# Kernel optimization log

Measured on AMD Instinct MI355X. Metric: run time of the kernel, lower is better.

Reference implementation:

```python
import jax, jax.numpy as jnp
import numpy as np

L = 2048
E = 1024
H = 16
D = E // H


def setup_inputs() -> dict:
    key = jax.random.key(0)
    ks = jax.random.split(key, 9)
    inp = {
        "values": jax.random.normal(ks[0], (L, E), dtype=jnp.float32),
        "keys": jax.random.normal(ks[1], (L, E), dtype=jnp.float32),
        "query": jax.random.normal(ks[2], (L, E), dtype=jnp.float32),
        "dist_matrix": jax.random.uniform(ks[3], (L, L), dtype=jnp.float32),
        "Wv": jax.random.normal(ks[4], (E, E), dtype=jnp.float32) * 0.02,
        "Wk": jax.random.normal(ks[5], (E, E), dtype=jnp.float32) * 0.02,
        "Wq": jax.random.normal(ks[6], (E, E), dtype=jnp.float32) * 0.02,
        "Wo": jax.random.normal(ks[7], (E, E), dtype=jnp.float32) * 0.02,
        "bo": jax.random.normal(ks[8], (E,), dtype=jnp.float32) * 0.02,
    }
    return inp


def reference(values, keys, query, dist_matrix, Wv, Wk, Wq, Wo, bo):
    # Linear projections (torch Linear: x @ W.T), then split heads: [L, H, D]
    v = (values @ Wv.T).reshape(L, H, D)
    k = (keys @ Wk.T).reshape(L, H, D)
    q = (query @ Wq.T).reshape(L, H, D)

    # energy: [H, Lq, Lk]
    energy = jnp.einsum("qhd,khd->hqk", q, k)

    # distance bias: zeros -> inf, then 1/(d+1); broadcast over heads
    dm = jnp.where(dist_matrix == 0, jnp.inf, dist_matrix)
    bias = 1.0 / (dm + 1.0)
    energy = energy + bias[None, :, :]

    attn = jax.nn.softmax(energy / jnp.sqrt(jnp.float32(E)), axis=2)

    out = jnp.einsum("hql,lhd->qhd", attn, v).reshape(L, H * D)
    return out @ Wo.T + bo
```

## Files before the change

### kernel.cpp

```cpp
#include <hip/hip_runtime.h>


#define L_SEQ 2048
#define E_DIM 1024
#define H_HEADS 16
#define D_HEAD 64
#define KSPLIT 4

typedef unsigned short u16;
typedef __attribute__((ext_vector_type(8))) short bf16x8;
typedef __attribute__((ext_vector_type(8))) unsigned short u16x8;
typedef __attribute__((ext_vector_type(4))) unsigned short u16x4;
typedef __attribute__((ext_vector_type(4))) float f32x4;

__device__ __forceinline__ float bf2f(u16 u) {
  union { unsigned int i; float f; } v; v.i = ((unsigned int)u) << 16; return v.f;
}
__device__ __forceinline__ u16 f2bf(float f) {
  union { float f; unsigned int i; } v; v.f = f;
  unsigned int u = v.i;
  u += 0x7FFFu + ((u >> 16) & 1u);
  return (u16)(u >> 16);
}

__global__ void cvt_all(const float* __restrict__ xq, const float* __restrict__ xk,
                        const float* __restrict__ xv,
                        const float* __restrict__ wq, const float* __restrict__ wk,
                        const float* __restrict__ wv, const float* __restrict__ wo,
                        const float* __restrict__ dist,
                        u16* oq, u16* ok, u16* ov,
                        u16* owq, u16* owk, u16* owv, u16* owo, u16* obias)
{
  size_t gid = (size_t)blockIdx.x * 256 + threadIdx.x;
  const size_t NQ = 524288;
  const size_t NW = 262144;
  const float* src; u16* dst; size_t off; bool isb = false;
  if      (gid <     NQ)           { src = xq;   dst = oq;    off = gid; }
  else if (gid < 2 * NQ)           { src = xk;   dst = ok;    off = gid - NQ; }
  else if (gid < 3 * NQ)           { src = xv;   dst = ov;    off = gid - 2 * NQ; }
  else if (gid < 3 * NQ + NW)      { src = wq;   dst = owq;   off = gid - 3 * NQ; }
  else if (gid < 3 * NQ + 2 * NW)  { src = wk;   dst = owk;   off = gid - 3 * NQ - NW; }
  else if (gid < 3 * NQ + 3 * NW)  { src = wv;   dst = owv;   off = gid - 3 * NQ - 2 * NW; }
  else if (gid < 3 * NQ + 4 * NW)  { src = wo;   dst = owo;   off = gid - 3 * NQ - 3 * NW; }
  else { src = dist; dst = obias; off = gid - 3 * NQ - 4 * NW; isb = true; }

  f32x4 v = *(const f32x4*)&src[off * 4];
  u16x4 o;
#pragma unroll
  for (int j = 0; j < 4; ++j) {
    float f = v[j];
    if (isb) f = (f == 0.f) ? 0.f : 1.f / (f + 1.f);
    o[j] = f2bf(f);
  }
  *(u16x4*)&dst[off * 4] = o;
}

#define TM 128
#define TN 128
#define BK 32
#define LDK 40

template<int OUTMODE>
__global__ __launch_bounds__(256, 2) void gemm_bt3b(
    const u16* __restrict__ A0, const u16* __restrict__ B0, void* __restrict__ C0,
    const u16* __restrict__ A1, const u16* __restrict__ B1, void* __restrict__ C1,
    const u16* __restrict__ A2, const u16* __restrict__ B2, void* __restrict__ C2,
    const float* __restrict__ bias, int M, int N, int K)
{
  const u16* A; const u16* B; void* C;
  if (blockIdx.z == 0)      { A = A0; B = B0; C = C0; }
  else if (blockIdx.z == 1) { A = A1; B = B1; C = C1; }
  else                      { A = A2; B = B2; C = C2; }

  __shared__ __align__(16) u16 As[TM][LDK];
  __shared__ __align__(16) u16 Bs[TN][LDK];

  const int m0 = blockIdx.y * TM;
  const int n0 = blockIdx.x * TN;
  const int t = threadIdx.x;
  const int wave = t >> 6;
  const int lane = t & 63;
  const int quad = lane >> 4;
  const int col  = lane & 15;
  const int wm = (wave >> 1) * 64;
  const int wn = (wave & 1) * 64;

  f32x4 acc[4][4];
#pragma unroll
  for (int i = 0; i < 4; ++i)
#pragma unroll
    for (int j = 0; j < 4; ++j) acc[i][j] = (f32x4){0.f, 0.f, 0.f, 0.f};

  for (int k0 = 0; k0 < K; k0 += BK) {
    __syncthreads();
#pragma unroll
    for (int s = 0; s < 2; ++s) {
      int idx = t + s * 256;
      int r  = idx >> 2;
      int c8 = (idx & 3) * 8;
      *(u16x8*)&As[r][c8] = *(const u16x8*)&A[(size_t)(m0 + r) * K + k0 + c8];
      *(u16x8*)&Bs[r][c8] = *(const u16x8*)&B[(size_t)(n0 + r) * K + k0 + c8];
    }
    __syncthreads();

    bf16x8 af[4], bfr[4];
#pragma unroll
    for (int i = 0; i < 4; ++i)
      af[i] = *(const bf16x8*)&As[wm + i * 16 + col][quad * 8];
#pragma unroll
    for (int j = 0; j < 4; ++j)
      bfr[j] = *(const bf16x8*)&Bs[wn + j * 16 + col][quad * 8];

#pragma unroll
    for (int i = 0; i < 4; ++i)
#pragma unroll
      for (int j = 0; j < 4; ++j)
        acc[i][j] = __builtin_amdgcn_mfma_f32_16x16x32_bf16(af[i], bfr[j], acc[i][j], 0, 0, 0);
  }

  const bool transC = (OUTMODE == 0) && (blockIdx.z == 2);
#pragma unroll
  for (int i = 0; i < 4; ++i) {
    int rowb = m0 + wm + i * 16 + quad * 4;
#pragma unroll
    for (int j = 0; j < 4; ++j) {
      int cn = n0 + wn + j * 16 + col;
      if (OUTMODE == 1) {
        float badd = bias ? bias[cn] : 0.f;
#pragma unroll
        for (int r = 0; r < 4; ++r)
          ((float*)C)[(size_t)(rowb + r) * N + cn] = acc[i][j][r] + badd;
      } else if (transC) {
        u16x4 pk;
#pragma unroll
        for (int r = 0; r < 4; ++r) pk[r] = f2bf(acc[i][j][r]);
        *(u16x4*)&((u16*)C)[(size_t)cn * M + rowb] = pk;
      } else {
#pragma unroll
        for (int r = 0; r < 4; ++r)
          ((u16*)C)[(size_t)(rowb + r) * N + cn] = f2bf(acc[i][j][r]);
      }
    }
  }
}

#define FK 64
#define LDV 72

__global__ __launch_bounds__(256, 5) void flash2(
    const u16* __restrict__ Q, const u16* __restrict__ Kp,
    const u16* __restrict__ Vt, const u16* __restrict__ Bb,
    u16* __restrict__ Op, float* __restrict__ lp)
{
  __shared__ __align__(16) u16 Ks[FK][LDV];
  __shared__ __align__(16) u16 Vs[D_HEAD][LDV];
  __shared__ __align__(16) u16 Ps[4][16][LDV];

  const int h  = blockIdx.y;
  const int q0 = blockIdx.x * 64;
  const int z  = blockIdx.z;
  const int hoff = h * D_HEAD;
  const int kbase = z * (L_SEQ / KSPLIT);
  const int t = threadIdx.x;
  const int wave = t >> 6;
  const int lane = t & 63;
  const int quad = lane >> 4;
  const int col  = lane & 15;

  bf16x8 qf[2];
  {
    const u16* qrow = Q + (size_t)(q0 + wave * 16 + col) * E_DIM + hoff;
    qf[0] = *(const bf16x8*)(qrow + quad * 8);
    qf[1] = *(const bf16x8*)(qrow + 32 + quad * 8);
  }

  float l_lane[4] = {0.f, 0.f, 0.f, 0.f};
  f32x4 oacc[4];
#pragma unroll
  for (int td = 0; td < 4; ++td) oacc[td] = (f32x4){0.f, 0.f, 0.f, 0.f};

  const int qrow_mine = q0 + wave * 16 + quad * 4;

  const int cst = t & 7, rst = t >> 3;
  for (int kt = 0; kt < L_SEQ / KSPLIT / FK; ++kt) {
    const int k0 = kbase + kt * FK;
    __syncthreads();
#pragma unroll
    for (int s = 0; s < 2; ++s) {
      int rr = rst + s * 32;
      *(u16x8*)&Ks[rr][cst * 8] = *(const u16x8*)&Kp[(size_t)(k0 + rr) * E_DIM + hoff + cst * 8];
      *(u16x8*)&Vs[rr][cst * 8] = *(const u16x8*)&Vt[(size_t)(hoff + rr) * L_SEQ + k0 + cst * 8];
    }
    float bias_v[4][4];
#pragma unroll
    for (int tt = 0; tt < 4; ++tt)
#pragma unroll
      for (int r = 0; r < 4; ++r)
        bias_v[tt][r] = bf2f(Bb[(size_t)(qrow_mine + r) * L_SEQ + k0 + tt * 16 + col]);
    __syncthreads();

    f32x4 sacc[4];
#pragma unroll
    for (int tt = 0; tt < 4; ++tt) {
      f32x4 a = (f32x4){0.f, 0.f, 0.f, 0.f};
      a = __builtin_amdgcn_mfma_f32_16x16x32_bf16(qf[0], *(const bf16x8*)&Ks[tt * 16 + col][quad * 8], a, 0, 0, 0);
      a = __builtin_amdgcn_mfma_f32_16x16x32_bf16(qf[1], *(const bf16x8*)&Ks[tt * 16 + col][32 + quad * 8], a, 0, 0, 0);
      sacc[tt] = a;
    }

#pragma unroll
    for (int tt = 0; tt < 4; ++tt) {
#pragma unroll
      for (int r = 0; r < 4; ++r) {
        float p = __expf((sacc[tt][r] + bias_v[tt][r]) * 0.03125f);
        l_lane[r] += p;
        Ps[wave][quad * 4 + r][tt * 16 + col] = f2bf(p);
      }
    }

#pragma unroll
    for (int kk = 0; kk < 2; ++kk) {
      bf16x8 pf = *(const bf16x8*)&Ps[wave][col][kk * 32 + quad * 8];
#pragma unroll
      for (int td = 0; td < 4; ++td) {
        bf16x8 vf = *(const bf16x8*)&Vs[td * 16 + col][kk * 32 + quad * 8];
        oacc[td] = __builtin_amdgcn_mfma_f32_16x16x32_bf16(pf, vf, oacc[td], 0, 0, 0);
      }
    }
  }

#pragma unroll
  for (int off = 1; off < 16; off <<= 1)
#pragma unroll
    for (int r = 0; r < 4; ++r) l_lane[r] += __shfl_xor(l_lane[r], off);

#pragma unroll
  for (int td = 0; td < 4; ++td)
#pragma unroll
    for (int r = 0; r < 4; ++r)
      Op[((size_t)z * L_SEQ + qrow_mine + r) * E_DIM + hoff + td * 16 + col] = f2bf(oacc[td][r]);

  if (col == 0) {
#pragma unroll
    for (int r = 0; r < 4; ++r)
      lp[((size_t)z * L_SEQ + qrow_mine + r) * H_HEADS + h] = l_lane[r];
  }
}

__global__ void merge_attn(const u16* __restrict__ Op, const float* __restrict__ lp,
                           u16* __restrict__ AOb)
{
  size_t gid = (size_t)blockIdx.x * 256 + threadIdx.x;
  size_t idx = gid * 4;
  int q = (int)(idx >> 10);
  int e = (int)(idx & 1023);
  int h = e >> 6;
  float o[4] = {0.f, 0.f, 0.f, 0.f};
  float lsum = 0.f;
#pragma unroll
  for (int s = 0; s < KSPLIT; ++s) {
    u16x4 pv = *(const u16x4*)&Op[((size_t)s * L_SEQ + q) * E_DIM + e];
#pragma unroll
    for (int j = 0; j < 4; ++j) o[j] += bf2f(pv[j]);
    lsum += lp[((size_t)s * L_SEQ + q) * H_HEADS + h];
  }
  float inv = 1.f / lsum;
  u16x4 pk;
#pragma unroll
  for (int j = 0; j < 4; ++j) pk[j] = f2bf(o[j] * inv);
  *(u16x4*)&AOb[idx] = pk;
}

extern "C" void kernel_launch(void* const* d_in, const int* in_sizes, int n_in,
                              void* d_out, int out_size, void* d_ws, size_t ws_size,
                              hipStream_t stream)
{
  const float* values = (const float*)d_in[0];
  const float* keys   = (const float*)d_in[1];
  const float* query  = (const float*)d_in[2];
  const float* dist   = (const float*)d_in[3];
  const float* Wv     = (const float*)d_in[4];
  const float* Wk     = (const float*)d_in[5];
  const float* Wq     = (const float*)d_in[6];
  const float* Wo     = (const float*)d_in[7];
  const float* bo     = (const float*)d_in[8];
  float* out = (float*)d_out;

  const size_t MB = (size_t)1 << 20;
  char* w = (char*)d_ws;
  u16* xq  = (u16*)(w + 0 * MB);
  u16* xk  = (u16*)(w + 4 * MB);
  u16* xv  = (u16*)(w + 8 * MB);
  u16* wqb = (u16*)(w + 12 * MB);
  u16* wkb = (u16*)(w + 14 * MB);
  u16* wvb = (u16*)(w + 16 * MB);
  u16* wob = (u16*)(w + 18 * MB);
  u16* Bb  = (u16*)(w + 20 * MB);
  u16* Qh  = (u16*)(w + 28 * MB);
  u16* Kh  = (u16*)(w + 32 * MB);
  u16* Vth = (u16*)(w + 36 * MB);
  u16* AOb = (u16*)(w + 40 * MB);
  float* lp = (float*)(w + 44 * MB);
  u16* Op  = (u16*)(w + 0 * MB);

  cvt_all<<<14336, 256, 0, stream>>>(query, keys, values, Wq, Wk, Wv, Wo, dist,
                                     xq, xk, xv, wqb, wkb, wvb, wob, Bb);

  dim3 gProj(E_DIM / TN, L_SEQ / TM, 3);
  gemm_bt3b<0><<<gProj, 256, 0, stream>>>(xq, wqb, Qh,
                                          xk, wkb, Kh,
                                          xv, wvb, Vth,
                                          nullptr, L_SEQ, E_DIM, E_DIM);

  dim3 gAttn(L_SEQ / 64, H_HEADS, KSPLIT);
  flash2<<<gAttn, 256, 0, stream>>>(Qh, Kh, Vth, Bb, Op, lp);

  merge_attn<<<(L_SEQ * E_DIM / 4) / 256, 256, 0, stream>>>(Op, lp, AOb);

  dim3 gOut(E_DIM / TN, L_SEQ / TM, 1);
  gemm_bt3b<1><<<gOut, 256, 0, stream>>>(AOb, wob, out,
                                         AOb, wob, out,
                                         AOb, wob, out,
                                         bo, L_SEQ, E_DIM, E_DIM);
}
```

Measured before the change: 236.1 us.

## Use direct global-to-LDS loads in GEMM and transpose score layout in attention

The projection GEMM now stages A/B tiles with global_load_lds directly into unpadded shared memory, avoiding a register round-trip. The attention kernel swaps MFMA operands so each lane holds one query row, which allows vectorized bias loads, packed bf16 stores of P and a single row-sum register per lane. Exponentials become exp2 with log2e folded into the precomputed bias and a fused multiply-add. Removing the LDS padding may bring back bank conflicts on the fragment reads, and the packing uses a simpler rounding.

```diff
diff --git a/kernel.cpp b/kernel.cpp
--- a/kernel.cpp
+++ b/kernel.cpp
@@ -8,19 +8,32 @@
 #define KSPLIT 4
 
 typedef unsigned short u16;
+typedef unsigned int u32;
 typedef __attribute__((ext_vector_type(8))) short bf16x8;
 typedef __attribute__((ext_vector_type(8))) unsigned short u16x8;
 typedef __attribute__((ext_vector_type(4))) unsigned short u16x4;
 typedef __attribute__((ext_vector_type(4))) float f32x4;
 
+#define C_LOG2E_32 0.045084220027780106f
+
 __device__ __forceinline__ float bf2f(u16 u) {
-  union { unsigned int i; float f; } v; v.i = ((unsigned int)u) << 16; return v.f;
+  union { u32 i; float f; } v; v.i = ((u32)u) << 16; return v.f;
 }
 __device__ __forceinline__ u16 f2bf(float f) {
-  union { float f; unsigned int i; } v; v.f = f;
-  unsigned int u = v.i;
+  union { float f; u32 i; } v; v.f = f;
+  u32 u = v.i;
   u += 0x7FFFu + ((u >> 16) & 1u);
   return (u16)(u >> 16);
+}
+__device__ __forceinline__ u32 pack_bf16_pair(float lo, float hi) {
+  union { float f; u32 u; } a, b;
+  a.f = lo; b.f = hi;
+  return __builtin_amdgcn_perm(b.u + 0x8000u, a.u + 0x8000u, 0x07060302u);
+}
+__device__ __forceinline__ void gload16(const u16* g, u16* l) {
+  __builtin_amdgcn_global_load_lds(
+      (const __attribute__((address_space(1))) u32*)g,
+      (__attribute__((address_space(3))) u32*)l, 16, 0, 0);
 }
 
 __global__ void cvt_all(const float* __restrict__ xq, const float* __restrict__ xk,
@@ -49,7 +62,7 @@
 #pragma unroll
   for (int j = 0; j < 4; ++j) {
     float f = v[j];
-    if (isb) f = (f == 0.f) ? 0.f : 1.f / (f + 1.f);
+    if (isb) f = (f == 0.f) ? 0.f : C_LOG2E_32 / (f + 1.f);
     o[j] = f2bf(f);
   }
   *(u16x4*)&dst[off * 4] = o;
@@ -58,7 +71,6 @@
 #define TM 128
 #define TN 128
 #define BK 32
-#define LDK 40
 
 template<int OUTMODE>
 __global__ __launch_bounds__(256, 2) void gemm_bt3b(
@@ -72,8 +84,8 @@
   else if (blockIdx.z == 1) { A = A1; B = B1; C = C1; }
   else                      { A = A2; B = B2; C = C2; }
 
-  __shared__ __align__(16) u16 As[TM][LDK];
-  __shared__ __align__(16) u16 Bs[TN][LDK];
+  __shared__ __align__(16) u16 As[TM][BK];
+  __shared__ __align__(16) u16 Bs[TN][BK];
 
   const int m0 = blockIdx.y * TM;
   const int n0 = blockIdx.x * TN;
@@ -85,6 +97,15 @@
   const int wm = (wave >> 1) * 64;
   const int wn = (wave & 1) * 64;
 
+  const int lr = lane >> 2;
+  const int lc = (lane & 3) * 8;
+  const u16* gA = A + (size_t)(m0 + wave * 32 + lr) * K + lc;
+  const u16* gB = B + (size_t)(n0 + wave * 32 + lr) * K + lc;
+  u16* lA0 = &As[wave * 32][0];
+  u16* lA1 = &As[wave * 32 + 16][0];
+  u16* lB0 = &Bs[wave * 32][0];
+  u16* lB1 = &Bs[wave * 32 + 16][0];
+
   f32x4 acc[4][4];
 #pragma unroll
   for (int i = 0; i < 4; ++i)
@@ -93,14 +114,10 @@
 
   for (int k0 = 0; k0 < K; k0 += BK) {
     __syncthreads();
-#pragma unroll
-    for (int s = 0; s < 2; ++s) {
-      int idx = t + s * 256;
-      int r  = idx >> 2;
-      int c8 = (idx & 3) * 8;
-      *(u16x8*)&As[r][c8] = *(const u16x8*)&A[(size_t)(m0 + r) * K + k0 + c8];
-      *(u16x8*)&Bs[r][c8] = *(const u16x8*)&B[(size_t)(n0 + r) * K + k0 + c8];
-    }
+    gload16(gA + k0, lA0);
+    gload16(gA + (size_t)16 * K + k0, lA1);
+    gload16(gB + k0, lB0);
+    gload16(gB + (size_t)16 * K + k0, lB1);
     __syncthreads();
 
     bf16x8 af[4], bfr[4];
@@ -147,7 +164,7 @@
 #define FK 64
 #define LDV 72
 
-__global__ __launch_bounds__(256, 5) void flash2(
+__global__ __launch_bounds__(256, 5) void flash3(
     const u16* __restrict__ Q, const u16* __restrict__ Kp,
     const u16* __restrict__ Vt, const u16* __restrict__ Bb,
     u16* __restrict__ Op, float* __restrict__ lp)
@@ -174,14 +191,14 @@
     qf[1] = *(const bf16x8*)(qrow + 32 + quad * 8);
   }
 
-  float l_lane[4] = {0.f, 0.f, 0.f, 0.f};
+  float l_lane = 0.f;
   f32x4 oacc[4];
 #pragma unroll
   for (int td = 0; td < 4; ++td) oacc[td] = (f32x4){0.f, 0.f, 0.f, 0.f};
 
-  const int qrow_mine = q0 + wave * 16 + quad * 4;
-
+  const u16* brow = Bb + (size_t)(q0 + wave * 16 + col) * L_SEQ;
   const int cst = t & 7, rst = t >> 3;
+
   for (int kt = 0; kt < L_SEQ / KSPLIT / FK; ++kt) {
     const int k0 = kbase + kt * FK;
     __syncthreads();
@@ -191,31 +208,30 @@
       *(u16x8*)&Ks[rr][cst * 8] = *(const u16x8*)&Kp[(size_t)(k0 + rr) * E_DIM + hoff + cst * 8];
       *(u16x8*)&Vs[rr][cst * 8] = *(const u16x8*)&Vt[(size_t)(hoff + rr) * L_SEQ + k0 + cst * 8];
     }
-    float bias_v[4][4];
-#pragma unroll
-    for (int tt = 0; tt < 4; ++tt)
-#pragma unroll
-      for (int r = 0; r < 4; ++r)
-        bias_v[tt][r] = bf2f(Bb[(size_t)(qrow_mine + r) * L_SEQ + k0 + tt * 16 + col]);
+    float pb[4][4];
+#pragma unroll
+    for (int tt = 0; tt < 4; ++tt) {
+      u16x4 bv = *(const u16x4*)&brow[k0 + tt * 16 + quad * 4];
+#pragma unroll
+      for (int r = 0; r < 4; ++r) pb[tt][r] = bf2f(bv[r]);
+    }
     __syncthreads();
 
-    f32x4 sacc[4];
 #pragma unroll
     for (int tt = 0; tt < 4; ++tt) {
       f32x4 a = (f32x4){0.f, 0.f, 0.f, 0.f};
-      a = __builtin_amdgcn_mfma_f32_16x16x32_bf16(qf[0], *(const bf16x8*)&Ks[tt * 16 + col][quad * 8], a, 0, 0, 0);
-      a = __builtin_amdgcn_mfma_f32_16x16x32_bf16(qf[1], *(const bf16x8*)&Ks[tt * 16 + col][32 + quad * 8], a, 0, 0, 0);
-      sacc[tt] = a;
-    }
-
-#pragma unroll
-    for (int tt = 0; tt < 4; ++tt) {
+      a = __builtin_amdgcn_mfma_f32_16x16x32_bf16(*(const bf16x8*)&Ks[tt * 16 + col][quad * 8], qf[0], a, 0, 0, 0);
+      a = __builtin_amdgcn_mfma_f32_16x16x32_bf16(*(const bf16x8*)&Ks[tt * 16 + col][32 + quad * 8], qf[1], a, 0, 0, 0);
+      float p[4];
 #pragma unroll
       for (int r = 0; r < 4; ++r) {
-        float p = __expf((sacc[tt][r] + bias_v[tt][r]) * 0.03125f);
-        l_lane[r] += p;
-        Ps[wave][quad * 4 + r][tt * 16 + col] = f2bf(p);
+        p[r] = __builtin_amdgcn_exp2f(fmaf(a[r], C_LOG2E_32, pb[tt][r]));
+        l_lane += p[r];
       }
+      uint2 w;
+      w.x = pack_bf16_pair(p[0], p[1]);
+      w.y = pack_bf16_pair(p[2], p[3]);
+      *(uint2*)&Ps[wave][col][tt * 16 + quad * 4] = w;
     }
 
 #pragma unroll
@@ -229,22 +245,17 @@
     }
   }
 
-#pragma unroll
-  for (int off = 1; off < 16; off <<= 1)
-#pragma unroll
-    for (int r = 0; r < 4; ++r) l_lane[r] += __shfl_xor(l_lane[r], off);
-
+  l_lane += __shfl_xor(l_lane, 16);
+  l_lane += __shfl_xor(l_lane, 32);
+  if (lane < 16)
+    lp[((size_t)z * L_SEQ + q0 + wave * 16 + lane) * H_HEADS + h] = l_lane;
+
+  const int qrow_mine = q0 + wave * 16 + quad * 4;
 #pragma unroll
   for (int td = 0; td < 4; ++td)
 #pragma unroll
     for (int r = 0; r < 4; ++r)
       Op[((size_t)z * L_SEQ + qrow_mine + r) * E_DIM + hoff + td * 16 + col] = f2bf(oacc[td][r]);
-
-  if (col == 0) {
-#pragma unroll
-    for (int r = 0; r < 4; ++r)
-      lp[((size_t)z * L_SEQ + qrow_mine + r) * H_HEADS + h] = l_lane[r];
-  }
 }
 
 __global__ void merge_attn(const u16* __restrict__ Op, const float* __restrict__ lp,
@@ -313,7 +324,7 @@
                                           nullptr, L_SEQ, E_DIM, E_DIM);
 
   dim3 gAttn(L_SEQ / 64, H_HEADS, KSPLIT);
-  flash2<<<gAttn, 256, 0, stream>>>(Qh, Kh, Vth, Bb, Op, lp);
+  flash3<<<gAttn, 256, 0, stream>>>(Qh, Kh, Vth, Bb, Op, lp);
 
   merge_attn<<<(L_SEQ * E_DIM / 4) / 256, 256, 0, stream>>>(Op, lp, AOb);
 
```

Result: faster. 218.2 us (-7.6%).
